# Kernel optimization log

Hardware: AMD Instinct MI355X
Metric: run time of the kernel (lower is better)

Reference implementation:

```python
import jax, jax.numpy as jnp
import numpy as np

HID = 2048
NH = 16
NKV = 4
HD = 256
ROT = 64  # partial_rotary_factor 0.25 * 256
EPS = 1e-6
B, S = 2, 2048


def rms_norm(x, w, eps=EPS):
    # Qwen3.5 RMSNorm: zero-init weight, (1 + w) scaling, fp32 compute
    xf = x.astype(jnp.float32)
    out = xf * jax.lax.rsqrt(jnp.mean(xf * xf, axis=-1, keepdims=True) + eps)
    return (out * (1.0 + w.astype(jnp.float32))).astype(x.dtype)


def rotate_half(x):
    x1, x2 = jnp.split(x, 2, axis=-1)
    return jnp.concatenate([-x2, x1], axis=-1)


def apply_partial_rope(q, k, cos, sin):
    # q,k: [b,h,s,d]; cos,sin: [b,s,rot] -> unsqueeze head dim
    c = cos[:, None, :, :]
    s = sin[:, None, :, :]
    q_rot, q_pass = q[..., :ROT], q[..., ROT:]
    k_rot, k_pass = k[..., :ROT], k[..., ROT:]
    q_rot = q_rot * c + rotate_half(q_rot) * s
    k_rot = k_rot * c + rotate_half(k_rot) * s
    return (jnp.concatenate([q_rot, q_pass], -1), jnp.concatenate([k_rot, k_pass], -1))


def setup_inputs() -> dict:
    key = jax.random.key(0)
    ks = jax.random.split(key, 10)
    hidden_states = jax.random.normal(ks[0], (B, S, HID), jnp.float32)
    # rotary embeddings over ROT dims (half freqs duplicated, HF-style)
    inv_freq = 1.0 / (10000.0 ** (np.arange(0, ROT, 2, dtype=np.float32) / ROT))
    t = np.arange(S, dtype=np.float32)
    freqs = np.outer(t, inv_freq)  # [S, ROT/2]
    emb = np.concatenate([freqs, freqs], axis=-1)  # [S, ROT]
    cos = jnp.broadcast_to(jnp.cos(emb)[None], (B, S, ROT)).astype(jnp.float32)
    sin = jnp.broadcast_to(jnp.sin(emb)[None], (B, S, ROT)).astype(jnp.float32)
    # additive causal mask
    m = jnp.where(jnp.tril(jnp.ones((S, S), bool)), 0.0, -1e9).astype(jnp.float32)
    attention_mask = jnp.broadcast_to(m[None, None], (B, 1, S, S))
    sc = 0.02
    Wq = jax.random.normal(ks[1], (HID, NH * HD * 2), jnp.float32) * sc
    Wk = jax.random.normal(ks[2], (HID, NKV * HD), jnp.float32) * sc
    Wv = jax.random.normal(ks[3], (HID, NKV * HD), jnp.float32) * sc
    Wo = jax.random.normal(ks[4], (NH * HD, HID), jnp.float32) * sc
    q_norm_w = jax.random.normal(ks[5], (HD,), jnp.float32) * sc
    k_norm_w = jax.random.normal(ks[6], (HD,), jnp.float32) * sc
    Wr = jax.random.normal(ks[7], (HID, 2 * HD), jnp.float32) * sc  # dynamic router
    return {"hidden_states": hidden_states, "cos": cos, "sin": sin,
            "attention_mask": attention_mask, "Wq": Wq, "Wk": Wk, "Wv": Wv,
            "Wo": Wo, "q_norm_w": q_norm_w, "k_norm_w": k_norm_w, "Wr": Wr}


def reference(hidden_states, cos, sin, attention_mask, Wq, Wk, Wv, Wo, q_norm_w, k_norm_w, Wr):
    b, s, _ = hidden_states.shape
    # dynamic router -> per-token virtual gates (inner_head for q/k, inner_head_v for v)
    vectors = jax.nn.sigmoid(hidden_states @ Wr)           # [b,s,2*HD]
    g_qk, g_v = jnp.split(vectors, 2, axis=-1)             # [b,s,HD] each
    # fused q projection -> query + sigmoid output gate
    qkv = (hidden_states @ Wq).reshape(b, s, NH, 2 * HD)
    q, gate = jnp.split(qkv, 2, axis=-1)                   # [b,s,NH,HD]
    gate = gate.reshape(b, s, NH * HD)
    k = (hidden_states @ Wk).reshape(b, s, NKV, HD)
    v = (hidden_states @ Wv).reshape(b, s, NKV, HD)
    # per-head RMSNorm before RoPE
    q = rms_norm(q, q_norm_w)
    k = rms_norm(k, k_norm_w)
    q = q.transpose(0, 2, 1, 3)                            # [b,NH,s,HD]
    k = k.transpose(0, 2, 1, 3)                            # [b,NKV,s,HD]
    v = v.transpose(0, 2, 1, 3)
    # virtual gating (inner_head): per-token per-channel gate within each head
    q = q * g_qk[:, None, :, :]
    k = k * g_qk[:, None, :, :]
    v = v * g_v[:, None, :, :]
    # partial RoPE on first ROT dims
    q, k = apply_partial_rope(q, k, cos, sin)
    # GQA: repeat kv heads
    n_rep = NH // NKV
    k = jnp.repeat(k, n_rep, axis=1)                       # [b,NH,s,HD]
    v = jnp.repeat(v, n_rep, axis=1)
    scores = jnp.einsum('bhqd,bhkd->bhqk', q, k) / jnp.sqrt(jnp.float32(HD))
    scores = scores + attention_mask
    attn = jax.nn.softmax(scores.astype(jnp.float32), axis=-1).astype(q.dtype)
    out = jnp.einsum('bhqk,bhkd->bhqd', attn, v)
    out = out.transpose(0, 2, 1, 3).reshape(b, s, NH * HD)
    out = out * jax.nn.sigmoid(gate)                       # sigmoid output gate
    return out @ Wo
```

## Files before the change

kernel.cpp:

```cpp
#include <hip/hip_runtime.h>

#define S_LEN 2048
#define NB    2
#define NH    16
#define NKV   4
#define HDIM  256
#define LW    10752

using bf16x8 = __attribute__((ext_vector_type(8))) short;
using s16x4  = __attribute__((ext_vector_type(4))) short;
using f32x4  = __attribute__((ext_vector_type(4))) float;

__device__ __forceinline__ float bf2f(short u){
  union { float f; unsigned u; } x; x.u = ((unsigned)(unsigned short)u) << 16; return x.f;
}
__device__ __forceinline__ short f2bf(float f){
  unsigned i = __builtin_bit_cast(unsigned, f);
  unsigned r = (i + 0x7fffu + ((i >> 16) & 1u)) >> 16;
  return (short)r;
}
__device__ __forceinline__ float sigm(float x){ return 1.0f / (1.0f + __expf(-x)); }

__device__ __forceinline__ void gload16(const short* g, short* lds){
  __builtin_amdgcn_global_load_lds((const __attribute__((address_space(1))) void*)g,
                                   (__attribute__((address_space(3))) void*)lds,
                                   16, 0, 0);
}

__global__ void k_cvt(const float* __restrict__ in, short* __restrict__ out, int n4){
  int i = blockIdx.x * blockDim.x + threadIdx.x;
  if (i >= n4) return;
  float4 v = ((const float4*)in)[i];
  s16x4 o;
  o[0] = f2bf(v.x); o[1] = f2bf(v.y); o[2] = f2bf(v.z); o[3] = f2bf(v.w);
  ((s16x4*)out)[i] = o;
}

__global__ void k_tcvt(const float* __restrict__ in, short* __restrict__ out, int R, int C){
  __shared__ float tile[32][33];
  int c0 = blockIdx.x * 32, r0 = blockIdx.y * 32;
  int tx = threadIdx.x, ty = threadIdx.y;
  #pragma unroll
  for (int i = ty; i < 32; i += 8)
    tile[i][tx] = in[(size_t)(r0 + i) * C + c0 + tx];
  __syncthreads();
  #pragma unroll
  for (int i = ty; i < 32; i += 8)
    out[(size_t)(c0 + i) * R + r0 + tx] = f2bf(tile[tx][i]);
}

__global__ void k_vt(const short* __restrict__ Ycat, short* __restrict__ VT){
  __shared__ short tile[32][33];
  int b = blockIdx.z >> 2, hk = blockIdx.z & 3;
  int s0 = blockIdx.x * 32, d0 = blockIdx.y * 32;
  int tx = threadIdx.x, ty = threadIdx.y;
  #pragma unroll
  for (int i = ty; i < 32; i += 8)
    tile[i][tx] = Ycat[(size_t)(b * S_LEN + s0 + i) * LW + 9216 + hk * 256 + d0 + tx];
  __syncthreads();
  #pragma unroll
  for (int i = ty; i < 32; i += 8)
    VT[(size_t)((b * NKV + hk) * HDIM + d0 + i) * S_LEN + s0 + tx] = tile[tx][i];
}

#define MFMA_(a, b, c) __builtin_amdgcn_mfma_f32_16x16x32_bf16(a, b, c, 0, 0, 0)
#define LDA_(buf, ks, mh, f) (*(const bf16x8*)&As[buf][ks][(wm*128 + (mh)*64 + (f)*16 + l15) * 32 + rdSlot])
#define LDB_(buf, ks, f)     (*(const bf16x8*)&Bs[buf][ks][(wn*64  + (f)*16 + l15) * 32 + rdSlot])
#define STAGE_A_(buf, ks, tile) { \
  gload16(aG0 + (size_t)(tile)*64 + (ks)*32, &As[buf][ks][w*512]); \
  gload16(aG1 + (size_t)(tile)*64 + (ks)*32, &As[buf][ks][4096 + w*512]); }
#define STAGE_B_(buf, ks, tile) { \
  gload16(bG0 + (size_t)(tile)*64 + (ks)*32, &Bs[buf][ks][w*512]); \
  gload16(bG1 + (size_t)(tile)*64 + (ks)*32, &Bs[buf][ks][4096 + w*512]); }
#define VM4 asm volatile("s_waitcnt vmcnt(4)" ::: "memory");
#define PH_(buf, ks, mh, LB, ...) { \
  bf16x8 a0 = LDA_(buf,ks,mh,0), a1 = LDA_(buf,ks,mh,1), a2 = LDA_(buf,ks,mh,2), a3 = LDA_(buf,ks,mh,3); \
  if (LB) { b0 = LDB_(buf,ks,0); b1 = LDB_(buf,ks,1); b2 = LDB_(buf,ks,2); b3 = LDB_(buf,ks,3); } \
  __VA_ARGS__ \
  __builtin_amdgcn_s_barrier(); \
  asm volatile("s_waitcnt lgkmcnt(0)" ::: "memory"); \
  __builtin_amdgcn_s_setprio(1); \
  acc[(mh)*4+0][0] = MFMA_(a0, b0, acc[(mh)*4+0][0]); \
  acc[(mh)*4+0][1] = MFMA_(a0, b1, acc[(mh)*4+0][1]); \
  acc[(mh)*4+0][2] = MFMA_(a0, b2, acc[(mh)*4+0][2]); \
  acc[(mh)*4+0][3] = MFMA_(a0, b3, acc[(mh)*4+0][3]); \
  acc[(mh)*4+1][0] = MFMA_(a1, b0, acc[(mh)*4+1][0]); \
  acc[(mh)*4+1][1] = MFMA_(a1, b1, acc[(mh)*4+1][1]); \
  acc[(mh)*4+1][2] = MFMA_(a1, b2, acc[(mh)*4+1][2]); \
  acc[(mh)*4+1][3] = MFMA_(a1, b3, acc[(mh)*4+1][3]); \
  acc[(mh)*4+2][0] = MFMA_(a2, b0, acc[(mh)*4+2][0]); \
  acc[(mh)*4+2][1] = MFMA_(a2, b1, acc[(mh)*4+2][1]); \
  acc[(mh)*4+2][2] = MFMA_(a2, b2, acc[(mh)*4+2][2]); \
  acc[(mh)*4+2][3] = MFMA_(a2, b3, acc[(mh)*4+2][3]); \
  acc[(mh)*4+3][0] = MFMA_(a3, b0, acc[(mh)*4+3][0]); \
  acc[(mh)*4+3][1] = MFMA_(a3, b1, acc[(mh)*4+3][1]); \
  acc[(mh)*4+3][2] = MFMA_(a3, b2, acc[(mh)*4+3][2]); \
  acc[(mh)*4+3][3] = MFMA_(a3, b3, acc[(mh)*4+3][3]); \
  __builtin_amdgcn_s_setprio(0); \
  __builtin_amdgcn_s_barrier(); }

template<int OUTF32>
__global__ __launch_bounds__(512) void k_gemm2(const short* __restrict__ A,
                                               const short* __restrict__ BT,
                                               void* __restrict__ C,
                                               int M, int N, int K, int gx)
{
  __shared__ __align__(16) short As[2][2][8192];
  __shared__ __align__(16) short Bs[2][2][8192];
  const int t = threadIdx.x, lane = t & 63, w = t >> 6;
  const int l15 = lane & 15;
  const int wm = w >> 2, wn = w & 3;
  const int rdSlot = (((lane >> 4) ^ (lane & 3)) * 8);

  const int nwg = gridDim.x;
  const int swz = (blockIdx.x & 7) * (nwg >> 3) + (blockIdx.x >> 3);
  const int m0 = (swz / gx) * 256, n0 = (swz % gx) * 256;

  const int sRow = w * 16 + (lane >> 2);
  const int sSwz = ((lane & 3) ^ ((lane >> 2) & 3)) * 8;
  const short* aG0 = A  + (size_t)(m0 + sRow) * K + sSwz;
  const short* aG1 = A  + (size_t)(m0 + 128 + sRow) * K + sSwz;
  const short* bG0 = BT + (size_t)(n0 + sRow) * K + sSwz;
  const short* bG1 = BT + (size_t)(n0 + 128 + sRow) * K + sSwz;

  f32x4 acc[8][4] = {};
  bf16x8 b0 = {}, b1 = {}, b2 = {}, b3 = {};

  STAGE_A_(0, 0, 0) STAGE_A_(0, 1, 0) STAGE_B_(0, 0, 0) STAGE_B_(0, 1, 0)
  STAGE_A_(1, 0, 1) STAGE_B_(1, 0, 1)
  asm volatile("s_waitcnt vmcnt(4)" ::: "memory");
  __builtin_amdgcn_s_barrier();

  const int nIt = K >> 7;
  for (int i = 0; i < nIt; ++i) {
    const int c = 2 * i;
    const bool st = (i + 1 < nIt);
    PH_(0, 0, 0, 1, STAGE_A_(1, 1, c + 1))
    PH_(0, 0, 1, 0, STAGE_B_(1, 1, c + 1))
    PH_(0, 1, 0, 1, if (st) STAGE_A_(0, 0, c + 2))
    PH_(0, 1, 1, 0, if (st) STAGE_B_(0, 0, c + 2) VM4)
    PH_(1, 0, 0, 1, if (st) STAGE_A_(0, 1, c + 2))
    PH_(1, 0, 1, 0, if (st) STAGE_B_(0, 1, c + 2))
    PH_(1, 1, 0, 1, if (st) STAGE_A_(1, 0, c + 3))
    PH_(1, 1, 1, 0, if (st) STAGE_B_(1, 0, c + 3) VM4)
  }

  #pragma unroll
  for (int ii = 0; ii < 8; ++ii)
    #pragma unroll
    for (int r = 0; r < 4; ++r) {
      const int row = m0 + wm * 128 + ii * 16 + (lane >> 4) * 4 + r;
      #pragma unroll
      for (int j = 0; j < 4; ++j) {
        const int col = n0 + wn * 64 + j * 16 + l15;
        const float v = acc[ii][j][r];
        if (OUTF32) ((float*)C)[(size_t)row * N + col] = v;
        else        ((short*)C)[(size_t)row * N + col] = f2bf(v);
      }
    }
}

__global__ __launch_bounds__(256) void k_post(short* __restrict__ Ycat,
    const float* __restrict__ cosb, const float* __restrict__ sinb,
    const float* __restrict__ qw, const float* __restrict__ kw)
{
  const int tok = blockIdx.x;
  const int lane = threadIdx.x & 63, w = threadIdx.x >> 6;
  const size_t rowb = (size_t)tok * LW;
  const int d0 = lane * 4;

  float gq[4], gv[4];
  {
    s16x4 a  = *(const s16x4*)&Ycat[rowb + 10240 + d0];
    s16x4 bq = *(const s16x4*)&Ycat[rowb + 10240 + 256 + d0];
    #pragma unroll
    for (int j = 0; j < 4; ++j){ gq[j] = sigm(bf2f(a[j])); gv[j] = sigm(bf2f(bq[j])); }
  }
  float c4[4] = {0,0,0,0}, s4[4] = {0,0,0,0};
  if (lane < 16) {
    float4 c = *(const float4*)&cosb[(size_t)tok * 64 + d0];
    float4 s = *(const float4*)&sinb[(size_t)tok * 64 + d0];
    c4[0]=c.x; c4[1]=c.y; c4[2]=c.z; c4[3]=c.w;
    s4[0]=s.x; s4[1]=s.y; s4[2]=s.z; s4[3]=s.w;
  }
  float4 qv4 = *(const float4*)&qw[d0];
  float4 kv4 = *(const float4*)&kw[d0];
  float qwa[4] = {qv4.x, qv4.y, qv4.z, qv4.w};
  float kwa[4] = {kv4.x, kv4.y, kv4.z, kv4.w};

  #pragma unroll
  for (int hi = 0; hi < 4; ++hi) {
    const int hh = w * 4 + hi;
    const size_t off = rowb + hh * 512 + d0;
    s16x4 v = *(const s16x4*)&Ycat[off];
    float x[4];
    #pragma unroll
    for (int j = 0; j < 4; ++j) x[j] = bf2f(v[j]);
    float ss = x[0]*x[0] + x[1]*x[1] + x[2]*x[2] + x[3]*x[3];
    #pragma unroll
    for (int o2 = 1; o2 < 64; o2 <<= 1) ss += __shfl_xor(ss, o2);
    float rr = rsqrtf(ss * (1.0f/256.0f) + 1e-6f);
    #pragma unroll
    for (int j = 0; j < 4; ++j) x[j] = x[j] * rr * (1.0f + qwa[j]) * gq[j];
    float p[4];
    #pragma unroll
    for (int j = 0; j < 4; ++j) p[j] = __shfl_xor(x[j], 8);
    if (lane < 8)       { for (int j = 0; j < 4; ++j) x[j] = x[j]*c4[j] - p[j]*s4[j]; }
    else if (lane < 16) { for (int j = 0; j < 4; ++j) x[j] = x[j]*c4[j] + p[j]*s4[j]; }
    s16x4 o;
    #pragma unroll
    for (int j = 0; j < 4; ++j) o[j] = f2bf(x[j]);
    *(s16x4*)&Ycat[off] = o;
  }
  {
    const size_t off = rowb + 8192 + w * 256 + d0;
    s16x4 v = *(const s16x4*)&Ycat[off];
    float x[4];
    #pragma unroll
    for (int j = 0; j < 4; ++j) x[j] = bf2f(v[j]);
    float ss = x[0]*x[0] + x[1]*x[1] + x[2]*x[2] + x[3]*x[3];
    #pragma unroll
    for (int o2 = 1; o2 < 64; o2 <<= 1) ss += __shfl_xor(ss, o2);
    float rr = rsqrtf(ss * (1.0f/256.0f) + 1e-6f);
    #pragma unroll
    for (int j = 0; j < 4; ++j) x[j] = x[j] * rr * (1.0f + kwa[j]) * gq[j];
    float p[4];
    #pragma unroll
    for (int j = 0; j < 4; ++j) p[j] = __shfl_xor(x[j], 8);
    if (lane < 8)       { for (int j = 0; j < 4; ++j) x[j] = x[j]*c4[j] - p[j]*s4[j]; }
    else if (lane < 16) { for (int j = 0; j < 4; ++j) x[j] = x[j]*c4[j] + p[j]*s4[j]; }
    s16x4 o;
    #pragma unroll
    for (int j = 0; j < 4; ++j) o[j] = f2bf(x[j]);
    *(s16x4*)&Ycat[off] = o;
  }
  {
    const size_t off = rowb + 9216 + w * 256 + d0;
    s16x4 v = *(const s16x4*)&Ycat[off];
    s16x4 o;
    #pragma unroll
    for (int j = 0; j < 4; ++j) o[j] = f2bf(bf2f(v[j]) * gv[j]);
    *(s16x4*)&Ycat[off] = o;
  }
}

#define ATT_STAGE(bb, jj) { \
  _Pragma("unroll") \
  for (int ri = 0; ri < 4; ++ri) \
    gload16(kSrc + (size_t)((jj) + ri*8) * LW, &Ks[bb][t*8 + ri*2048]); \
  _Pragma("unroll") \
  for (int ri = 0; ri < 4; ++ri) \
    gload16(vSrc + (jj) + (size_t)(ri*64) * S_LEN, &Vs[bb][t*8 + ri*2048]); }

__global__ __launch_bounds__(256) void k_attn(const short* __restrict__ Ycat,
                                              const short* __restrict__ VT,
                                              short* __restrict__ AO)
{
  __shared__ __align__(16) short Ks[2][8192];
  __shared__ __align__(16) short Vs[2][8192];
  __shared__ __align__(16) short Ps[4][512];

  const int t = threadIdx.x, lane = t & 63, w = t >> 6;
  const int l15 = lane & 15, g = lane >> 4;
  const int id = blockIdx.x;
  const int xcd = id & 7, widx = id >> 3;
  const int b = xcd >> 2, hk = xcd & 3;
  const int h = hk * 4 + (widx & 3);
  const int q0 = (31 - (widx >> 2)) * 64;
  const int qg = q0 + w * 16 + l15;
  const float SC2 = 0.09016844f;

  bf16x8 qf[8];
  {
    const size_t qb = ((size_t)(b * S_LEN) + qg) * LW + h * 512 + g * 8;
    #pragma unroll
    for (int kk = 0; kk < 8; ++kk)
      qf[kk] = *(const bf16x8*)&Ycat[qb + kk * 32];
  }
  asm volatile("s_waitcnt vmcnt(0)" ::: "memory");

  const int kRow = t >> 5;
  const int kColS = ((((t & 31) * 16) ^ ((kRow & 7) << 4)) >> 1);
  const int vRow = t >> 2;
  const int vColS = ((((t & 3) * 16) ^ ((vRow & 3) << 4)) >> 1);
  const short* kSrc = Ycat + ((size_t)(b * S_LEN) + kRow) * LW + 8192 + hk * 256 + kColS;
  const short* vSrc = VT + ((size_t)((b * NKV + hk) * HDIM + vRow)) * S_LEN + vColS;

  f32x4 oacc[16] = {};
  float m_r = -1e30f, l_r = 0.0f;

  const int nt = (q0 >> 5) + 2;
  ATT_STAGE(0, 0)
  int buf = 0;
  char* Pw = (char*)Ps[w] + l15 * 64;
  const int pswz = (l15 & 3) << 4;

  for (int ti = 0; ti < nt; ++ti) {
    const int j0 = ti * 32;
    const int jn = (ti + 1 < nt) ? j0 + 32 : 0;
    ATT_STAGE(buf ^ 1, jn)
    asm volatile("s_waitcnt vmcnt(8)" ::: "memory");
    __builtin_amdgcn_s_barrier();

    if (j0 <= q0 + w * 16 + 15) {
      f32x4 sa[2] = {};
      #pragma unroll
      for (int kk = 0; kk < 8; ++kk) {
        #pragma unroll
        for (int c = 0; c < 2; ++c) {
          const int row = c * 16 + l15;
          bf16x8 kf = *(const bf16x8*)((const char*)Ks[buf] + row * 512
                       + ((kk * 64 + g * 16) ^ ((l15 & 7) << 4)));
          sa[c] = __builtin_amdgcn_mfma_f32_16x16x32_bf16(kf, qf[kk], sa[c], 0, 0, 0);
        }
      }
      float s[8];
      #pragma unroll
      for (int c = 0; c < 2; ++c)
        #pragma unroll
        for (int r = 0; r < 4; ++r) s[c * 4 + r] = sa[c][r];
      if (j0 + 31 > qg) {
        #pragma unroll
        for (int c = 0; c < 2; ++c)
          #pragma unroll
          for (int r = 0; r < 4; ++r)
            if (j0 + c * 16 + g * 4 + r > qg) s[c * 4 + r] = -1e30f;
      }
      float mx = s[0];
      #pragma unroll
      for (int i = 1; i < 8; ++i) mx = fmaxf(mx, s[i]);
      mx = fmaxf(mx, __shfl_xor(mx, 16));
      mx = fmaxf(mx, __shfl_xor(mx, 32));
      if (!__all(mx - m_r <= 128.0f)) {
        const float mnew = fmaxf(m_r, mx);
        const float alpha = exp2f((m_r - mnew) * SC2);
        l_r *= alpha;
        #pragma unroll
        for (int jb = 0; jb < 16; ++jb)
          #pragma unroll
          for (int r = 0; r < 4; ++r) oacc[jb][r] *= alpha;
        m_r = mnew;
      }
      float p[8], rs = 0.0f;
      #pragma unroll
      for (int i = 0; i < 8; ++i) { p[i] = exp2f((s[i] - m_r) * SC2); rs += p[i]; }
      rs += __shfl_xor(rs, 16);
      rs += __shfl_xor(rs, 32);
      l_r += rs;
      #pragma unroll
      for (int c = 0; c < 2; ++c) {
        uint2 u;
        u.x = (unsigned short)f2bf(p[c*4+0]) | ((unsigned)(unsigned short)f2bf(p[c*4+1]) << 16);
        u.y = (unsigned short)f2bf(p[c*4+2]) | ((unsigned)(unsigned short)f2bf(p[c*4+3]) << 16);
        *(uint2*)(Pw + ((c * 32 + 8 * g) ^ pswz)) = u;
      }
      bf16x8 pa = *(const bf16x8*)(Pw + ((16 * g) ^ pswz));
      #pragma unroll
      for (int jb = 0; jb < 16; ++jb) {
        const int vrow = jb * 16 + l15;
        bf16x8 vf = *(const bf16x8*)((const char*)Vs[buf] + vrow * 64
                     + ((16 * g) ^ ((l15 & 3) << 4)));
        oacc[jb] = __builtin_amdgcn_mfma_f32_16x16x32_bf16(vf, pa, oacc[jb], 0, 0, 0);
      }
    }
    __builtin_amdgcn_s_barrier();
    buf ^= 1;
  }
  asm volatile("s_waitcnt vmcnt(0)" ::: "memory");

  const float linv = 1.0f / l_r;
  const size_t gb = ((size_t)(b * S_LEN) + qg) * LW + h * 512 + 256;
  const size_t ob = ((size_t)(b * S_LEN) + qg) * 4096 + h * 256;
  #pragma unroll
  for (int jb = 0; jb < 16; ++jb) {
    const int d0 = jb * 16 + g * 4;
    s16x4 gt = *(const s16x4*)&Ycat[gb + d0];
    s16x4 o;
    #pragma unroll
    for (int r = 0; r < 4; ++r)
      o[r] = f2bf(oacc[jb][r] * linv * sigm(bf2f(gt[r])));
    *(s16x4*)&AO[ob + d0] = o;
  }
}

extern "C" void kernel_launch(void* const* d_in, const int* in_sizes, int n_in,
                              void* d_out, int out_size, void* d_ws, size_t ws_size,
                              hipStream_t stream) {
  const float* X    = (const float*)d_in[0];
  const float* cosb = (const float*)d_in[1];
  const float* sinb = (const float*)d_in[2];
  const float* Wq   = (const float*)d_in[4];
  const float* Wk   = (const float*)d_in[5];
  const float* Wv   = (const float*)d_in[6];
  const float* Wo   = (const float*)d_in[7];
  const float* qw   = (const float*)d_in[8];
  const float* kw   = (const float*)d_in[9];
  const float* Wr   = (const float*)d_in[10];

  short* Xb    = (short*)d_ws;
  short* WcatT = Xb    +  8388608;
  short* AO    = WcatT;
  short* WoT   = WcatT + 22020096;
  short* Ycat  = WoT   +  8388608;
  short* VT    = Ycat  + 44040192;

  dim3 tb(32, 8);
  k_cvt<<<8192, 256, 0, stream>>>(X, Xb, 2097152);
  k_tcvt<<<dim3(256, 64), tb, 0, stream>>>(Wq, WcatT,                      2048, 8192);
  k_tcvt<<<dim3( 32, 64), tb, 0, stream>>>(Wk, WcatT + (size_t)8192*2048,  2048, 1024);
  k_tcvt<<<dim3( 32, 64), tb, 0, stream>>>(Wv, WcatT + (size_t)9216*2048,  2048, 1024);
  k_tcvt<<<dim3( 16, 64), tb, 0, stream>>>(Wr, WcatT + (size_t)10240*2048, 2048,  512);
  k_tcvt<<<dim3( 64,128), tb, 0, stream>>>(Wo, WoT,                        4096, 2048);

  k_gemm2<0><<<672, 512, 0, stream>>>(Xb, WcatT, Ycat, 4096, 10752, 2048, 42);
  k_post<<<4096, 256, 0, stream>>>(Ycat, cosb, sinb, qw, kw);
  k_vt<<<dim3(64, 8, 8), tb, 0, stream>>>(Ycat, VT);
  k_attn<<<1024, 256, 0, stream>>>(Ycat, VT, AO);
  k_gemm2<1><<<128, 512, 0, stream>>>(AO, WoT, d_out, 4096, 2048, 4096, 8);
}
```

Before: 551.8 us.

## Merge weight transposes, reorder GEMM tiles, change LDS swizzle, rebalance attention schedule

Five weight transpose-convert launches become one kernel that picks its source matrix from the block index. This cuts launch overhead and tail gaps between the small launches. The QKV GEMM now walks tiles column-major (M fastest, gx=16) so that workgroups sharing a weight tile run close together. The LDS swizzle pattern used for staging and reading is changed, presumably to reduce bank conflicts. Attention query-block ordering is interleaved across heavy and light causal blocks to balance load per XCD. Together these change several unrelated scheduling aspects, and the swizzle change must stay consistent between the write and read sides.

```diff
diff --git a/kernel.cpp b/kernel.cpp
--- a/kernel.cpp
+++ b/kernel.cpp
@@ -36,17 +36,28 @@
   ((s16x4*)out)[i] = o;
 }
 
-__global__ void k_tcvt(const float* __restrict__ in, short* __restrict__ out, int R, int C){
+__global__ void k_wt(const float* __restrict__ Wq, const float* __restrict__ Wk,
+                     const float* __restrict__ Wv, const float* __restrict__ Wr,
+                     const float* __restrict__ Wo, short* __restrict__ WcatT,
+                     short* __restrict__ WoT)
+{
   __shared__ float tile[32][33];
-  int c0 = blockIdx.x * 32, r0 = blockIdx.y * 32;
-  int tx = threadIdx.x, ty = threadIdx.y;
+  const int id = blockIdx.x;
+  const float* src; short* dst; int R, C, Ct, local;
+  if (id < 16384)      { src = Wq; dst = WcatT;                      R = 2048; C = 8192; Ct = 256; local = id; }
+  else if (id < 18432) { src = Wk; dst = WcatT + (size_t)8192*2048;  R = 2048; C = 1024; Ct =  32; local = id - 16384; }
+  else if (id < 20480) { src = Wv; dst = WcatT + (size_t)9216*2048;  R = 2048; C = 1024; Ct =  32; local = id - 18432; }
+  else if (id < 21504) { src = Wr; dst = WcatT + (size_t)10240*2048; R = 2048; C =  512; Ct =  16; local = id - 20480; }
+  else                 { src = Wo; dst = WoT;                        R = 4096; C = 2048; Ct =  64; local = id - 21504; }
+  const int c0 = (local % Ct) * 32, r0 = (local / Ct) * 32;
+  const int tx = threadIdx.x, ty = threadIdx.y;
   #pragma unroll
   for (int i = ty; i < 32; i += 8)
-    tile[i][tx] = in[(size_t)(r0 + i) * C + c0 + tx];
+    tile[i][tx] = src[(size_t)(r0 + i) * C + c0 + tx];
   __syncthreads();
   #pragma unroll
   for (int i = ty; i < 32; i += 8)
-    out[(size_t)(c0 + i) * R + r0 + tx] = f2bf(tile[tx][i]);
+    dst[(size_t)(c0 + i) * R + r0 + tx] = f2bf(tile[tx][i]);
 }
 
 __global__ void k_vt(const short* __restrict__ Ycat, short* __restrict__ VT){
@@ -99,7 +110,7 @@
   __builtin_amdgcn_s_setprio(0); \
   __builtin_amdgcn_s_barrier(); }
 
-template<int OUTF32>
+template<int OUTF32, int CM>
 __global__ __launch_bounds__(512) void k_gemm2(const short* __restrict__ A,
                                                const short* __restrict__ BT,
                                                void* __restrict__ C,
@@ -110,14 +121,15 @@
   const int t = threadIdx.x, lane = t & 63, w = t >> 6;
   const int l15 = lane & 15;
   const int wm = w >> 2, wn = w & 3;
-  const int rdSlot = (((lane >> 4) ^ (lane & 3)) * 8);
+  const int rdSlot = (((lane >> 4) ^ ((lane >> 1) & 3)) * 8);
 
   const int nwg = gridDim.x;
   const int swz = (blockIdx.x & 7) * (nwg >> 3) + (blockIdx.x >> 3);
-  const int m0 = (swz / gx) * 256, n0 = (swz % gx) * 256;
+  const int m0 = (CM ? (swz % gx) : (swz / gx)) * 256;
+  const int n0 = (CM ? (swz / gx) : (swz % gx)) * 256;
 
   const int sRow = w * 16 + (lane >> 2);
-  const int sSwz = ((lane & 3) ^ ((lane >> 2) & 3)) * 8;
+  const int sSwz = ((lane & 3) ^ ((lane >> 3) & 3)) * 8;
   const short* aG0 = A  + (size_t)(m0 + sRow) * K + sSwz;
   const short* aG1 = A  + (size_t)(m0 + 128 + sRow) * K + sSwz;
   const short* bG0 = BT + (size_t)(n0 + sRow) * K + sSwz;
@@ -266,7 +278,9 @@
   const int xcd = id & 7, widx = id >> 3;
   const int b = xcd >> 2, hk = xcd & 3;
   const int h = hk * 4 + (widx & 3);
-  const int q0 = (31 - (widx >> 2)) * 64;
+  const int x = widx >> 2, qq = x & 7, jj = x >> 3;
+  const int qsel = (jj == 0) ? 31 - qq : (jj == 1) ? 16 + qq : (jj == 2) ? 15 - qq : qq;
+  const int q0 = qsel * 64;
   const int qg = q0 + w * 16 + l15;
   const float SC2 = 0.09016844f;
 
@@ -406,15 +420,11 @@
 
   dim3 tb(32, 8);
   k_cvt<<<8192, 256, 0, stream>>>(X, Xb, 2097152);
-  k_tcvt<<<dim3(256, 64), tb, 0, stream>>>(Wq, WcatT,                      2048, 8192);
-  k_tcvt<<<dim3( 32, 64), tb, 0, stream>>>(Wk, WcatT + (size_t)8192*2048,  2048, 1024);
-  k_tcvt<<<dim3( 32, 64), tb, 0, stream>>>(Wv, WcatT + (size_t)9216*2048,  2048, 1024);
-  k_tcvt<<<dim3( 16, 64), tb, 0, stream>>>(Wr, WcatT + (size_t)10240*2048, 2048,  512);
-  k_tcvt<<<dim3( 64,128), tb, 0, stream>>>(Wo, WoT,                        4096, 2048);
-
-  k_gemm2<0><<<672, 512, 0, stream>>>(Xb, WcatT, Ycat, 4096, 10752, 2048, 42);
+  k_wt<<<29696, tb, 0, stream>>>(Wq, Wk, Wv, Wr, Wo, WcatT, WoT);
+
+  k_gemm2<0, 1><<<672, 512, 0, stream>>>(Xb, WcatT, Ycat, 4096, 10752, 2048, 16);
   k_post<<<4096, 256, 0, stream>>>(Ycat, cosb, sinb, qw, kw);
   k_vt<<<dim3(64, 8, 8), tb, 0, stream>>>(Ycat, VT);
   k_attn<<<1024, 256, 0, stream>>>(Ycat, VT, AO);
-  k_gemm2<1><<<128, 512, 0, stream>>>(AO, WoT, d_out, 4096, 2048, 4096, 8);
-}
+  k_gemm2<1, 0><<<128, 512, 0, stream>>>(AO, WoT, d_out, 4096, 2048, 4096, 8);
+}
```

Result: faster. 537.2 us (-2.7%).
